# Performance work log

Hardware: AMD Instinct MI355X
Metric: run time of the kernel (lower is better)

The kernel has to match this reference:

```python
import jax, jax.numpy as jnp
import numpy as np

N, K, D = 65536, 1024, 256
COMMIT = 0.25
EPS = 1e-12


def setup_inputs() -> dict:
    key = jax.random.key(0)
    kx, kw = jax.random.split(key)
    x = jax.random.normal(kx, (N, D), dtype=jnp.float32)
    # nn.Embedding weight init: uniform(-1/vector_num, 1/vector_num)
    weight = jax.random.uniform(kw, (K, D), dtype=jnp.float32,
                                minval=-1.0 / K, maxval=1.0 / K)
    return {"x": x, "weight": weight}


def reference(x, weight):
    distances = (jnp.sum(x * x, axis=1, keepdims=True)
                 + jnp.sum(weight * weight, axis=1)
                 - 2.0 * (x @ weight.T))
    vector_indices = jnp.argmin(distances, axis=1)              # [N]
    quantized = weight[vector_indices]                          # gather == one-hot @ weight

    e_latent_loss = jnp.mean((jax.lax.stop_gradient(quantized) - x) ** 2)
    q_latent_loss = jnp.mean((quantized - jax.lax.stop_gradient(x)) ** 2)
    quant_loss = q_latent_loss + COMMIT * e_latent_loss

    # straight-through estimator
    quantized_out = x + jax.lax.stop_gradient(quantized - x)

    # utilization: counts of each code (== column sums of one-hot encodings)
    counts = jnp.zeros((K,), x.dtype).at[vector_indices].add(1.0)
    util_loss = jnp.mean(jnp.abs(counts - x.shape[0] / K))

    # compactness: 2 * mean of pairwise euclidean distances among codebook rows
    sq = jnp.sum(weight * weight, axis=1)
    pd2 = sq[:, None] + sq[None, :] - 2.0 * (weight @ weight.T)  # [K, K]
    iu = jnp.triu(jnp.ones((K, K), bool), 1)
    pd = jnp.sqrt(jnp.maximum(jnp.where(iu, pd2, 1.0), EPS))
    n_pairs = K * (K - 1) // 2
    compact_loss = 2.0 * jnp.sum(jnp.where(iu, pd, 0.0)) / n_pairs

    return quantized_out, quant_loss, util_loss, compact_loss, vector_indices
```

## Files before the change

### kernel.cpp

```cpp
#include <hip/hip_runtime.h>
#include <math.h>

#define NROWS 65536
#define KCODES 1024
#define DDIM 256
#define ND_TOT (NROWS * DDIM)

#define WS_IDX      0
#define WS_COUNTS   262144
#define WS_SW       266240
#define WS_PARTQ    532480
#define WS_PARTP    536576
#define WS_FLAGCNT  540672
#define WS_FLAGLIST 540928
#define WS_WH       803072
#define WS_WL       1327360

typedef float f32x4 __attribute__((ext_vector_type(4)));
typedef short bf16x8 __attribute__((ext_vector_type(8)));

__device__ inline unsigned short f2bf(float f) {
  unsigned u = __float_as_uint(f);
  u += 0x7FFFu + ((u >> 16) & 1u);
  return (unsigned short)(u >> 16);
}
__device__ inline float bf2f(unsigned short h) {
  return __uint_as_float(((unsigned)h) << 16);
}

__device__ inline void gload16(const void* g, void* l) {
  __builtin_amdgcn_global_load_lds((const __attribute__((address_space(1))) void*)g,
                                   (__attribute__((address_space(3))) void*)l, 16, 0, 0);
}

__global__ __launch_bounds__(256) void vq_prep(const float* __restrict__ x,
                                               const float* __restrict__ w,
                                               unsigned short* __restrict__ xh,
                                               unsigned short* __restrict__ xl,
                                               float* __restrict__ sw,
                                               unsigned short* __restrict__ wh,
                                               unsigned short* __restrict__ wl,
                                               int* __restrict__ counts,
                                               int* __restrict__ flagCnt) {
#pragma clang fp contract(off)
  const int b = blockIdx.x;
  const int t = threadIdx.x;
  if (b >= 2048) {
    const int lane = t & 63, wv = t >> 6;
    const int row = (b - 2048) * 4 + wv;
    const float* src = w + (size_t)row * DDIM;
    float4 v4 = *(const float4*)&src[lane * 4];
    float fv[4] = {v4.x, v4.y, v4.z, v4.w};
    union { unsigned short us[4]; uint2 v; } ph, pl;
#pragma unroll
    for (int e = 0; e < 4; ++e) {
      unsigned short h = f2bf(fv[e]);
      ph.us[e] = h;
      pl.us[e] = f2bf(fv[e] - bf2f(h));
    }
    *(uint2*)&wh[(size_t)row * DDIM + lane * 4] = ph.v;
    *(uint2*)&wl[(size_t)row * DDIM + lane * 4] = pl.v;
    float acc = 0.f;
    if (lane < 16) {
      const float* p = src + ((lane >> 3) & 1) * 128 + (lane & 7);
      float v = p[0];
      acc = v * v;
      for (int k = 1; k < 16; ++k) { float vv = p[k * 8]; float e = vv * vv; acc = acc + e; }
    }
    acc = acc + __shfl_xor(acc, 1);
    acc = acc + __shfl_xor(acc, 2);
    acc = acc + __shfl_xor(acc, 4);
    const float hb = __shfl(acc, 8);
    if (lane == 0) sw[row] = acc + hb;
    return;
  }
  if (b == 0) {
#pragma unroll
    for (int j = 0; j < 4; ++j) counts[j * 256 + t] = 0;
    if (t == 0) flagCnt[0] = 0;
  }
  const size_t tid = (size_t)b * 256 + t;
  float4 a[4], c[4];
#pragma unroll
  for (int g = 0; g < 4; ++g) {
    const size_t e = ((size_t)g * 524288 + tid) * 8;
    a[g] = *(const float4*)&x[e];
    c[g] = *(const float4*)&x[e + 4];
  }
#pragma unroll
  for (int g = 0; g < 4; ++g) {
    const size_t e = ((size_t)g * 524288 + tid) * 8;
    float fv[8] = {a[g].x, a[g].y, a[g].z, a[g].w, c[g].x, c[g].y, c[g].z, c[g].w};
    union { unsigned short us[8]; uint4 v; } ph, pl;
#pragma unroll
    for (int k = 0; k < 8; ++k) {
      unsigned short h = f2bf(fv[k]);
      ph.us[k] = h;
      pl.us[k] = f2bf(fv[k] - bf2f(h));
    }
    *(uint4*)&xh[e] = ph.v;
    *(uint4*)&xl[e] = pl.v;
  }
}

#define TRM 128
#define BKM 64
#define REPAIR_T 1.5e-4f

__global__ __launch_bounds__(256, 2) void vq_argmin_mfma(
    const unsigned short* __restrict__ xh, const unsigned short* __restrict__ xl,
    const unsigned short* __restrict__ wh, const unsigned short* __restrict__ wl,
    const float* __restrict__ sw,
    int* __restrict__ idxOut, float* __restrict__ idxOutF,
    int* __restrict__ flagCnt, int* __restrict__ flagList) {
  __shared__ __align__(16) unsigned short lds_xh[TRM * BKM];
  __shared__ __align__(16) unsigned short lds_xl[TRM * BKM];
  __shared__ __align__(16) unsigned short lds_wh[TRM * BKM];
  __shared__ __align__(16) unsigned short lds_wl[TRM * BKM];
  __shared__ __align__(16) float sws[KCODES];
  __shared__ float mrgB1[TRM][2];
  __shared__ float mrgB2[TRM][2];
  __shared__ int   mrgI[TRM][2];

  const int t = threadIdx.x;
  const int lane = t & 63, wv = t >> 6;
  const int wr = wv >> 1, wc = wv & 1;
  const int row0 = blockIdx.x * TRM;

  { f32x4 v = ((const f32x4*)sw)[t]; ((f32x4*)sws)[t] = v; }

  const int laneRow = lane >> 3;
  const int srcswz = ((lane & 7) * 16) ^ ((laneRow & 7) << 4);
  const char* xhB = (const char*)xh;
  const char* xlB = (const char*)xl;
  const char* whB = (const char*)wh;
  const char* wlB = (const char*)wl;

  float b1[16], b2[16];
  int bi[16];
#pragma unroll
  for (int s = 0; s < 16; ++s) { b1[s] = 3.4e38f; b2[s] = 3.4e38f; bi[s] = 0; }

  for (int ct = 0; ct < KCODES / TRM; ++ct) {
    f32x4 acc[4][4];
#pragma unroll
    for (int i = 0; i < 4; ++i)
#pragma unroll
      for (int j = 0; j < 4; ++j) acc[i][j] = (f32x4){0.f, 0.f, 0.f, 0.f};

    for (int dt = 0; dt < 4; ++dt) {
      __syncthreads();
#pragma unroll
      for (int i = 0; i < 4; ++i) {
        const int rb = wv * 32 + i * 8;
        const size_t gox = (size_t)(row0 + rb + laneRow) * 512 + (size_t)(dt * 128 + srcswz);
        gload16(xhB + gox, (char*)lds_xh + rb * 128);
        gload16(xlB + gox, (char*)lds_xl + rb * 128);
        const size_t gow = (size_t)(ct * 128 + rb + laneRow) * 512 + (size_t)(dt * 128 + srcswz);
        gload16(whB + gow, (char*)lds_wh + rb * 128);
        gload16(wlB + gow, (char*)lds_wl + rb * 128);
      }
      __syncthreads();

#pragma unroll
      for (int kh = 0; kh < 2; ++kh) {
        const int kb = kh * 64 + (lane >> 4) * 16;
        bf16x8 ah[4], al[4];
#pragma unroll
        for (int i = 0; i < 4; ++i) {
          const int r = wr * 64 + i * 16 + (lane & 15);
          const int off = r * 128 + (kb ^ ((r & 7) << 4));
          ah[i] = *(const bf16x8*)((const char*)lds_xh + off);
          al[i] = *(const bf16x8*)((const char*)lds_xl + off);
        }
#pragma unroll
        for (int j = 0; j < 4; ++j) {
          const int c = wc * 64 + j * 16 + (lane & 15);
          const int off = c * 128 + (kb ^ ((c & 7) << 4));
          bf16x8 bh = *(const bf16x8*)((const char*)lds_wh + off);
          bf16x8 bl = *(const bf16x8*)((const char*)lds_wl + off);
#pragma unroll
          for (int i = 0; i < 4; ++i) {
            acc[i][j] = __builtin_amdgcn_mfma_f32_16x16x32_bf16(ah[i], bh, acc[i][j], 0, 0, 0);
            acc[i][j] = __builtin_amdgcn_mfma_f32_16x16x32_bf16(ah[i], bl, acc[i][j], 0, 0, 0);
            acc[i][j] = __builtin_amdgcn_mfma_f32_16x16x32_bf16(al[i], bh, acc[i][j], 0, 0, 0);
          }
        }
      }
    }

#pragma unroll
    for (int j = 0; j < 4; ++j) {
      const int colbase = ct * 128 + wc * 64 + j * 16 + (lane & 15);
      const float swv = sws[colbase];
#pragma unroll
      for (int i = 0; i < 4; ++i)
#pragma unroll
        for (int q = 0; q < 4; ++q) {
          const int s = i * 4 + q;
          const float e = fmaf(-2.f, acc[i][j][q], swv);
          const bool c1 = e < b1[s];
          b2[s] = c1 ? b1[s] : fminf(b2[s], e);
          bi[s] = c1 ? colbase : bi[s];
          b1[s] = fminf(b1[s], e);
        }
    }
  }

#pragma unroll
  for (int off = 1; off < 16; off <<= 1) {
#pragma unroll
    for (int s = 0; s < 16; ++s) {
      const float ob1 = __shfl_xor(b1[s], off);
      const float ob2 = __shfl_xor(b2[s], off);
      const int oi = __shfl_xor(bi[s], off);
      const float hi = fmaxf(b1[s], ob1);
      const bool take = ob1 < b1[s];
      b1[s] = fminf(b1[s], ob1);
      b2[s] = fminf(hi, fminf(b2[s], ob2));
      bi[s] = take ? oi : bi[s];
    }
  }
  if ((lane & 15) == 0) {
#pragma unroll
    for (int i = 0; i < 4; ++i)
#pragma unroll
      for (int q = 0; q < 4; ++q) {
        const int s = i * 4 + q;
        const int r = wr * 64 + i * 16 + (lane >> 4) * 4 + q;
        mrgB1[r][wc] = b1[s]; mrgB2[r][wc] = b2[s]; mrgI[r][wc] = bi[s];
      }
  }
  __syncthreads();
  if (t < TRM) {
    const float b1a = mrgB1[t][0], b1b = mrgB1[t][1];
    const float b2a = mrgB2[t][0], b2b = mrgB2[t][1];
    const bool take = b1b < b1a;
    const float b1f = fminf(b1a, b1b);
    const float b2f = fminf(fmaxf(b1a, b1b), fminf(b2a, b2b));
    const int idxf = take ? mrgI[t][1] : mrgI[t][0];
    const int grow = row0 + t;
    idxOut[grow] = idxf;
    idxOutF[grow] = (float)idxf;
    const bool flag = (b2f - b1f) < REPAIR_T;
    unsigned long long m = __ballot(flag);
    int base2 = 0;
    if ((t & 63) == 0) base2 = atomicAdd(flagCnt, __popcll(m));
    base2 = __shfl(base2, 0);
    if (flag) flagList[base2 + __popcll(m & ((1ull << (t & 63)) - 1ull))] = grow;
  }
}

#define RPB 8
__global__ __launch_bounds__(256) void vq_repair_compact(
    const float* __restrict__ x, const float* __restrict__ w,
    const float* __restrict__ sw,
    const int* __restrict__ flagCnt, const int* __restrict__ flagList,
    int* __restrict__ idxOut, float* __restrict__ idxOutF,
    float* __restrict__ partialP) {
  const int t = threadIdx.x;
  const int lane = t & 63, wvid = t >> 6;
  if (blockIdx.x >= 1024) {
    const int i = blockIdx.x - 1024;
    __shared__ float wi[DDIM];
    wi[t] = w[(size_t)i * DDIM + t];
    __syncthreads();
    float swi = sw[i];
    double s = 0.0;
    for (int j = i + 1 + t; j < KCODES; j += 256) {
      const float4* wj = (const float4*)(w + (size_t)j * DDIM);
      const float4* wi4 = (const float4*)wi;
      float acc = 0.f;
#pragma unroll 8
      for (int d4 = 0; d4 < DDIM / 4; ++d4) {
        float4 a = wi4[d4];
        float4 b = wj[d4];
        acc += a.x * b.x + a.y * b.y + a.z * b.z + a.w * b.w;
      }
      float pd2 = (swi + sw[j]) - 2.0f * acc;
      s += (double)sqrtf(fmaxf(pd2, 1e-12f));
    }
    for (int off = 32; off > 0; off >>= 1) s += __shfl_down(s, off);
    __shared__ double redc[4];
    if (lane == 0) redc[wvid] = s;
    __syncthreads();
    if (t == 0)
      partialP[i] = (float)(redc[0] + redc[1] + redc[2] + redc[3]);
    return;
  }
  __shared__ float xrow[RPB][DDIM];
  __shared__ float sxsh[RPB];
  __shared__ float redD[RPB][4];
  __shared__ int   redI[RPB][4];
  const int cnt = flagCnt[0];
  for (int base = blockIdx.x * RPB; base < cnt; base += 1024 * RPB) {
    const int nr = min(RPB, cnt - base);
    __syncthreads();
    for (int r = 0; r < nr; ++r)
      xrow[r][t] = x[(size_t)flagList[base + r] * DDIM + t];
    __syncthreads();
    if (t < nr) {
#pragma clang fp contract(off)
      float halves[2];
#pragma unroll
      for (int h = 0; h < 2; ++h) {
        const float* p = &xrow[t][h * 128];
        float acc[8];
#pragma unroll
        for (int j = 0; j < 8; ++j) { float v = p[j]; acc[j] = v * v; }
        for (int i = 8; i < 128; i += 8) {
#pragma unroll
          for (int j = 0; j < 8; ++j) { float v = p[i + j]; float e = v * v; acc[j] = acc[j] + e; }
        }
        halves[h] = ((acc[0] + acc[1]) + (acc[2] + acc[3])) + ((acc[4] + acc[5]) + (acc[6] + acc[7]));
      }
      sxsh[t] = halves[0] + halves[1];
    }
    __syncthreads();
    float bD[RPB]; int bI[RPB];
#pragma unroll
    for (int r = 0; r < RPB; ++r) { bD[r] = 3.4e38f; bI[r] = 0x7fffffff; }
    for (int g = 0; g < 4; ++g) {
      const int c = g * 256 + t;
      const float4* wrp = (const float4*)(w + (size_t)c * DDIM);
      float acc[RPB];
#pragma unroll
      for (int r = 0; r < RPB; ++r) acc[r] = 0.f;
      for (int d4 = 0; d4 < DDIM / 4; ++d4) {
        const float4 wv = wrp[d4];
#pragma unroll
        for (int e = 0; e < 4; ++e) {
          const float wvx = (e == 0) ? wv.x : (e == 1) ? wv.y : (e == 2) ? wv.z : wv.w;
#pragma unroll
          for (int r = 0; r < RPB; ++r) acc[r] = fmaf(xrow[r][d4 * 4 + e], wvx, acc[r]);
        }
      }
      const float swc = sw[c];
#pragma unroll
      for (int r = 0; r < RPB; ++r) {
        const float tt = sxsh[r] + swc;
        const float dist = tt - 2.0f * acc[r];
        if (dist < bD[r]) { bD[r] = dist; bI[r] = c; }
      }
    }
#pragma unroll
    for (int off = 32; off > 0; off >>= 1) {
#pragma unroll
      for (int r = 0; r < RPB; ++r) {
        const float od = __shfl_down(bD[r], off);
        const int oi = __shfl_down(bI[r], off);
        if (od < bD[r] || (od == bD[r] && oi < bI[r])) { bD[r] = od; bI[r] = oi; }
      }
    }
    if (lane == 0) {
#pragma unroll
      for (int r = 0; r < RPB; ++r) { redD[r][wvid] = bD[r]; redI[r][wvid] = bI[r]; }
    }
    __syncthreads();
    if (t < nr) {
      float bb = redD[t][0]; int bix = redI[t][0];
#pragma unroll
      for (int k = 1; k < 4; ++k) {
        const float od = redD[t][k]; const int oi = redI[t][k];
        if (od < bb || (od == bb && oi < bix)) { bb = od; bix = oi; }
      }
      const int row = flagList[base + t];
      idxOut[row] = bix;
      idxOutF[row] = (float)bix;
    }
  }
}

__global__ __launch_bounds__(256) void vq_quantize(const float* __restrict__ x,
                                                   const float* __restrict__ w,
                                                   const int* __restrict__ idxArr,
                                                   float* __restrict__ qout,
                                                   int* __restrict__ counts,
                                                   float* __restrict__ partialQ) {
  const int wave = threadIdx.x >> 6;
  const int lane = threadIdx.x & 63;
  const int base = blockIdx.x * 64 + wave * 16;
  float s = 0.f;
#pragma unroll
  for (int rg = 0; rg < 4; ++rg) {
    int idx4[4];
#pragma unroll
    for (int r = 0; r < 4; ++r) idx4[r] = idxArr[base + rg * 4 + r];
    float4 xv[4], qv[4];
#pragma unroll
    for (int r = 0; r < 4; ++r) {
      xv[r] = ((const float4*)(x + (size_t)(base + rg * 4 + r) * DDIM))[lane];
      qv[r] = ((const float4*)(w + (size_t)idx4[r] * DDIM))[lane];
    }
#pragma unroll
    for (int r = 0; r < 4; ++r) {
      const int row = base + rg * 4 + r;
      float dx = qv[r].x - xv[r].x, dy = qv[r].y - xv[r].y;
      float dz = qv[r].z - xv[r].z, dw = qv[r].w - xv[r].w;
      float4 o;
      o.x = xv[r].x + dx; o.y = xv[r].y + dy; o.z = xv[r].z + dz; o.w = xv[r].w + dw;
      ((float4*)(qout + (size_t)row * DDIM))[lane] = o;
      s += dx * dx + dy * dy + dz * dz + dw * dw;
      if (lane == 0) atomicAdd(&counts[idx4[r]], 1);
    }
  }
  double d = s;
  for (int off = 32; off > 0; off >>= 1) d += __shfl_down(d, off);
  __shared__ double red[4];
  if (lane == 0) red[wave] = d;
  __syncthreads();
  if (threadIdx.x == 0)
    partialQ[blockIdx.x] = (float)(red[0] + red[1] + red[2] + red[3]);
}

__global__ __launch_bounds__(1024) void vq_final(const float* __restrict__ partialQ,
                                                 const float* __restrict__ partialP,
                                                 const int* __restrict__ counts,
                                                 float* __restrict__ out) {
  const int t = threadIdx.x;
  const int lane = t & 63, wave = t >> 6;
  double q = (double)partialQ[t];
  double p = (double)partialP[t];
  double u = (double)fabsf((float)counts[t] - 64.0f);
  for (int off = 32; off > 0; off >>= 1) {
    q += __shfl_down(q, off);
    p += __shfl_down(p, off);
    u += __shfl_down(u, off);
  }
  __shared__ double redQ[16], redP[16], redU[16];
  if (lane == 0) { redQ[wave] = q; redP[wave] = p; redU[wave] = u; }
  __syncthreads();
  if (t == 0) {
    double sq = 0, sp = 0, su = 0;
    for (int j = 0; j < 16; ++j) { sq += redQ[j]; sp += redP[j]; su += redU[j]; }
    float m = (float)(sq / 16777216.0);
    out[ND_TOT] = m + 0.25f * m;
    out[ND_TOT + 1] = (float)(su / 1024.0);
    out[ND_TOT + 2] = (float)(2.0 * sp / 523776.0);
  }
}

extern "C" void kernel_launch(void* const* d_in, const int* in_sizes, int n_in,
                              void* d_out, int out_size, void* d_ws, size_t ws_size,
                              hipStream_t stream) {
  const float* x = (const float*)d_in[0];
  const float* w = (const float*)d_in[1];
  float* out = (float*)d_out;

  char* ws = (char*)d_ws;
  int* wsIdx    = (int*)(ws + WS_IDX);
  int* counts   = (int*)(ws + WS_COUNTS);
  float* swv    = (float*)(ws + WS_SW);
  float* partQ  = (float*)(ws + WS_PARTQ);
  float* partP  = (float*)(ws + WS_PARTP);
  int* flagCnt  = (int*)(ws + WS_FLAGCNT);
  int* flagList = (int*)(ws + WS_FLAGLIST);
  unsigned short* whS = (unsigned short*)(ws + WS_WH);
  unsigned short* wlS = (unsigned short*)(ws + WS_WL);

  unsigned short* xhS = (unsigned short*)d_out;
  unsigned short* xlS = xhS + (size_t)ND_TOT;

  vq_prep<<<2304, 256, 0, stream>>>(x, w, xhS, xlS, swv, whS, wlS, counts, flagCnt);
  vq_argmin_mfma<<<NROWS / TRM, 256, 0, stream>>>(xhS, xlS, whS, wlS, swv,
                                                  wsIdx, out + ND_TOT + 3, flagCnt, flagList);
  vq_repair_compact<<<2048, 256, 0, stream>>>(x, w, swv, flagCnt, flagList,
                                              wsIdx, out + ND_TOT + 3, partP);
  vq_quantize<<<1024, 256, 0, stream>>>(x, w, wsIdx, out, counts, partQ);
  vq_final<<<1, 1024, 0, stream>>>(partQ, partP, counts, out);
}
```

Measured before the change: 263.2 us.

## Keep x fragments in registers and give each wave all 128 codes per tile

The argmin kernel now loads each wave's 32 rows of split-bf16 x (hi and lo) straight from global memory into registers once, instead of restaging x through LDS for every code tile and depth slice. Each wave now covers 32 rows against all 128 codes of the tile rather than a 64x64 quadrant, so the final cross-wave merge of best and second-best is dropped. This removes repeated x global loads and LDS traffic, but it adds about 64 VGPRs of held x fragments and doubles the W fragments each wave reads from LDS per MFMA. That raises register pressure under the 2-blocks-per-SM launch bound.

Measured after the change: 249.8 us. 1.05x faster.

```diff
diff --git a/kernel.cpp b/kernel.cpp
--- a/kernel.cpp
+++ b/kernel.cpp
@@ -113,49 +113,55 @@
     const float* __restrict__ sw,
     int* __restrict__ idxOut, float* __restrict__ idxOutF,
     int* __restrict__ flagCnt, int* __restrict__ flagList) {
-  __shared__ __align__(16) unsigned short lds_xh[TRM * BKM];
-  __shared__ __align__(16) unsigned short lds_xl[TRM * BKM];
   __shared__ __align__(16) unsigned short lds_wh[TRM * BKM];
   __shared__ __align__(16) unsigned short lds_wl[TRM * BKM];
   __shared__ __align__(16) float sws[KCODES];
-  __shared__ float mrgB1[TRM][2];
-  __shared__ float mrgB2[TRM][2];
-  __shared__ int   mrgI[TRM][2];
+  __shared__ float mrgB1[TRM];
+  __shared__ float mrgB2[TRM];
+  __shared__ int   mrgI[TRM];
 
   const int t = threadIdx.x;
   const int lane = t & 63, wv = t >> 6;
-  const int wr = wv >> 1, wc = wv & 1;
   const int row0 = blockIdx.x * TRM;
 
   { f32x4 v = ((const f32x4*)sw)[t]; ((f32x4*)sws)[t] = v; }
 
   const int laneRow = lane >> 3;
   const int srcswz = ((lane & 7) * 16) ^ ((laneRow & 7) << 4);
-  const char* xhB = (const char*)xh;
-  const char* xlB = (const char*)xl;
   const char* whB = (const char*)wh;
   const char* wlB = (const char*)wl;
 
-  float b1[16], b2[16];
-  int bi[16];
-#pragma unroll
-  for (int s = 0; s < 16; ++s) { b1[s] = 3.4e38f; b2[s] = 3.4e38f; bi[s] = 0; }
+  bf16x8 ah[2][8], al[2][8];
+  {
+    const int rbase = row0 + wv * 32 + (lane & 15);
+    const int kof = ((lane >> 4) & 3) * 8;
+#pragma unroll
+    for (int i = 0; i < 2; ++i)
+#pragma unroll
+      for (int ks = 0; ks < 8; ++ks) {
+        const size_t e = (size_t)(rbase + i * 16) * DDIM + (size_t)(ks * 32 + kof);
+        ah[i][ks] = *(const bf16x8*)&xh[e];
+        al[i][ks] = *(const bf16x8*)&xl[e];
+      }
+  }
+
+  float b1[8], b2[8];
+  int bi[8];
+#pragma unroll
+  for (int s = 0; s < 8; ++s) { b1[s] = 3.4e38f; b2[s] = 3.4e38f; bi[s] = 0; }
 
   for (int ct = 0; ct < KCODES / TRM; ++ct) {
-    f32x4 acc[4][4];
-#pragma unroll
-    for (int i = 0; i < 4; ++i)
-#pragma unroll
-      for (int j = 0; j < 4; ++j) acc[i][j] = (f32x4){0.f, 0.f, 0.f, 0.f};
+    f32x4 acc[2][8];
+#pragma unroll
+    for (int i = 0; i < 2; ++i)
+#pragma unroll
+      for (int j = 0; j < 8; ++j) acc[i][j] = (f32x4){0.f, 0.f, 0.f, 0.f};
 
     for (int dt = 0; dt < 4; ++dt) {
       __syncthreads();
 #pragma unroll
       for (int i = 0; i < 4; ++i) {
         const int rb = wv * 32 + i * 8;
-        const size_t gox = (size_t)(row0 + rb + laneRow) * 512 + (size_t)(dt * 128 + srcswz);
-        gload16(xhB + gox, (char*)lds_xh + rb * 128);
-        gload16(xlB + gox, (char*)lds_xl + rb * 128);
         const size_t gow = (size_t)(ct * 128 + rb + laneRow) * 512 + (size_t)(dt * 128 + srcswz);
         gload16(whB + gow, (char*)lds_wh + rb * 128);
         gload16(wlB + gow, (char*)lds_wl + rb * 128);
@@ -164,37 +170,30 @@
 
 #pragma unroll
       for (int kh = 0; kh < 2; ++kh) {
-        const int kb = kh * 64 + (lane >> 4) * 16;
-        bf16x8 ah[4], al[4];
-#pragma unroll
-        for (int i = 0; i < 4; ++i) {
-          const int r = wr * 64 + i * 16 + (lane & 15);
-          const int off = r * 128 + (kb ^ ((r & 7) << 4));
-          ah[i] = *(const bf16x8*)((const char*)lds_xh + off);
-          al[i] = *(const bf16x8*)((const char*)lds_xl + off);
-        }
-#pragma unroll
-        for (int j = 0; j < 4; ++j) {
-          const int c = wc * 64 + j * 16 + (lane & 15);
+        const int kb = kh * 64 + ((lane >> 4) & 3) * 16;
+        const int ks = dt * 2 + kh;
+#pragma unroll
+        for (int j = 0; j < 8; ++j) {
+          const int c = j * 16 + (lane & 15);
           const int off = c * 128 + (kb ^ ((c & 7) << 4));
           bf16x8 bh = *(const bf16x8*)((const char*)lds_wh + off);
           bf16x8 bl = *(const bf16x8*)((const char*)lds_wl + off);
 #pragma unroll
-          for (int i = 0; i < 4; ++i) {
-            acc[i][j] = __builtin_amdgcn_mfma_f32_16x16x32_bf16(ah[i], bh, acc[i][j], 0, 0, 0);
-            acc[i][j] = __builtin_amdgcn_mfma_f32_16x16x32_bf16(ah[i], bl, acc[i][j], 0, 0, 0);
-            acc[i][j] = __builtin_amdgcn_mfma_f32_16x16x32_bf16(al[i], bh, acc[i][j], 0, 0, 0);
+          for (int i = 0; i < 2; ++i) {
+            acc[i][j] = __builtin_amdgcn_mfma_f32_16x16x32_bf16(ah[i][ks], bh, acc[i][j], 0, 0, 0);
+            acc[i][j] = __builtin_amdgcn_mfma_f32_16x16x32_bf16(ah[i][ks], bl, acc[i][j], 0, 0, 0);
+            acc[i][j] = __builtin_amdgcn_mfma_f32_16x16x32_bf16(al[i][ks], bh, acc[i][j], 0, 0, 0);
           }
         }
       }
     }
 
 #pragma unroll
-    for (int j = 0; j < 4; ++j) {
-      const int colbase = ct * 128 + wc * 64 + j * 16 + (lane & 15);
+    for (int j = 0; j < 8; ++j) {
+      const int colbase = ct * 128 + j * 16 + (lane & 15);
       const float swv = sws[colbase];
 #pragma unroll
-      for (int i = 0; i < 4; ++i)
+      for (int i = 0; i < 2; ++i)
 #pragma unroll
         for (int q = 0; q < 4; ++q) {
           const int s = i * 4 + q;
@@ -210,7 +209,7 @@
 #pragma unroll
   for (int off = 1; off < 16; off <<= 1) {
 #pragma unroll
-    for (int s = 0; s < 16; ++s) {
+    for (int s = 0; s < 8; ++s) {
       const float ob1 = __shfl_xor(b1[s], off);
       const float ob2 = __shfl_xor(b2[s], off);
       const int oi = __shfl_xor(bi[s], off);
@@ -223,22 +222,19 @@
   }
   if ((lane & 15) == 0) {
 #pragma unroll
-    for (int i = 0; i < 4; ++i)
+    for (int i = 0; i < 2; ++i)
 #pragma unroll
       for (int q = 0; q < 4; ++q) {
         const int s = i * 4 + q;
-        const int r = wr * 64 + i * 16 + (lane >> 4) * 4 + q;
-        mrgB1[r][wc] = b1[s]; mrgB2[r][wc] = b2[s]; mrgI[r][wc] = bi[s];
+        const int r = wv * 32 + i * 16 + ((lane >> 4) & 3) * 4 + q;
+        mrgB1[r] = b1[s]; mrgB2[r] = b2[s]; mrgI[r] = bi[s];
       }
   }
   __syncthreads();
   if (t < TRM) {
-    const float b1a = mrgB1[t][0], b1b = mrgB1[t][1];
-    const float b2a = mrgB2[t][0], b2b = mrgB2[t][1];
-    const bool take = b1b < b1a;
-    const float b1f = fminf(b1a, b1b);
-    const float b2f = fminf(fmaxf(b1a, b1b), fminf(b2a, b2b));
-    const int idxf = take ? mrgI[t][1] : mrgI[t][0];
+    const float b1f = mrgB1[t];
+    const float b2f = mrgB2[t];
+    const int idxf = mrgI[t];
     const int grow = row0 + t;
     idxOut[grow] = idxf;
     idxOutF[grow] = (float)idxf;
```
